# Kernel tuning notes

Hardware: AMD Instinct MI355X
Metric: run time of the kernel (lower is better)

Reference implementation:

```python
import jax, jax.numpy as jnp
import numpy as np

R, H, K, C = 8, 8, 4096, 128  # residual stages, subvectors, codebook size, subvector dim
B, S = 2, 2048


def setup_inputs() -> dict:
    key = jax.random.key(0)
    k1, k2 = jax.random.split(key)
    x = jax.random.normal(k1, (B, S, H * C), dtype=jnp.float32)
    codebook = jax.random.normal(k2, (R, H, K, C), dtype=jnp.float32) * 0.1
    return {"x": x, "codebook": codebook}


def _encode(x, codebook):
    b, s, f = x.shape
    # x.view(b,s,8,2,64).transpose(3,4).flatten(2)  -> interleave the two 64-dim halves per head
    xp = x.reshape(b, s, 8, 2, 64).transpose(0, 1, 2, 4, 3).reshape(b, s, f)
    prescale = jnp.linalg.norm(xp, axis=-1, keepdims=True)  # (b,s,1)
    xn = xp / prescale
    # (b s) h c  -> permute to (h, N, c)
    t0 = xn.reshape(b * s, H, C).transpose(1, 0, 2)  # (H, N, C)

    def step(t, cb_r):
        # cb_r: (H, K, C). Squared-euclidean argmin == torch.cdist argmin (sqrt is monotone,
        # and the ||t||^2 term is constant over k so it is dropped).
        d = jnp.sum(cb_r * cb_r, axis=-1)[:, None, :] - 2.0 * jnp.einsum('hnc,hkc->hnk', t, cb_r)
        idx = jnp.argmin(d, axis=-1)  # (H, N)
        q = jnp.take_along_axis(cb_r, idx[..., None], axis=1)  # (H, N, C)
        return t - q, idx.astype(jnp.int32)

    _, codes = jax.lax.scan(step, t0, codebook)  # codes: (R, H, N)
    return codes, prescale


def _decode(codes, prescale, codebook):
    # gather codebook entries: (R, H, N, C)
    g = jnp.take_along_axis(codebook, codes[..., None], axis=2)
    n = codes.shape[2]
    # permute(0,2,1,3).flatten(-2).sum(0): (R,N,H*C) summed over residual stages
    rec = g.transpose(0, 2, 1, 3).reshape(R, n, H * C).sum(0)  # (N, H*C)
    b = prescale.shape[0]
    return rec.reshape(b, -1, H * C) * prescale


def reference(x, codebook):
    codes, prescale = _encode(x, codebook)
    return _decode(codes, prescale, codebook)
```

## Files before the change

kernel.cpp:

```cpp
#include <hip/hip_runtime.h>

#define R_STAGES 8
#define H_HEADS  8
#define K_CODES  4096
#define C_DIM    128
#define N_TOK    4096
#define FEAT     1024
#define HKC      (H_HEADS * K_CODES * C_DIM)

#define MARGIN   1.2e-2f
#define WCAP     384
#define TMS      260
#define NTILE    64
#define NPH      (K_CODES / NTILE)
#define TPB      64

typedef _Float16 half8  __attribute__((ext_vector_type(8)));
typedef _Float16 half4v __attribute__((ext_vector_type(4)));
typedef float    f32x4  __attribute__((ext_vector_type(4)));

#define MFMA16(A, B, C) __builtin_amdgcn_mfma_f32_16x16x32_f16((A), (B), (C), 0, 0, 0)

__device__ __forceinline__ void glds16(const _Float16* g, _Float16* l) {
    __builtin_amdgcn_global_load_lds(
        (const __attribute__((address_space(1))) void*)g,
        (__attribute__((address_space(3))) void*)l, 16, 0, 0);
}


__global__ void kc_prep(const float* __restrict__ x, float* __restrict__ t,
                        float* __restrict__ ps) {
    int n = blockIdx.x;
    const float* xr = x + (size_t)n * FEAT;

    double ss = 0.0;
    for (int i = threadIdx.x; i < FEAT; i += 256) {
        float v = xr[i];
        ss += (double)v * (double)v;
    }
    for (int off = 32; off > 0; off >>= 1) ss += __shfl_down(ss, off);

    __shared__ double sred[4];
    __shared__ float s_p;
    int wid = threadIdx.x >> 6, lane = threadIdx.x & 63;
    if (lane == 0) sred[wid] = ss;
    __syncthreads();
    if (threadIdx.x == 0) {
        double tot = sred[0] + sred[1] + sred[2] + sred[3];
        float p = (float)sqrt(tot);
        ps[n] = p;
        s_p = p;
    }
    __syncthreads();
    float p = s_p;

    for (int i = threadIdx.x; i < FEAT; i += 256) {
        int c = i & 127;
        float v = xr[(i & ~127) + ((c & 1) << 6) + (c >> 1)];
        size_t o = ((size_t)(i >> 7) * N_TOK + n) * C_DIM + c;
        t[o] = v / p;
    }
}

__global__ void kc_cvtn(const float* __restrict__ cb, _Float16* __restrict__ cb16,
                        float* __restrict__ cn) {
    int w = (blockIdx.x << 2) + (threadIdx.x >> 6);
    int lane = threadIdx.x & 63;
    const float* row = cb + (size_t)w * C_DIM;
    float a = row[lane], b = row[lane + 64];
    _Float16* dr = cb16 + (size_t)w * C_DIM;
    dr[lane]      = (_Float16)a;
    dr[lane + 64] = (_Float16)b;
    double s = (double)a * a + (double)b * b;
    for (int off = 32; off > 0; off >>= 1) s += __shfl_down(s, off);
    if (lane == 0) cn[w] = (float)s;
}

__device__ __forceinline__ void stage_body(
    const float* __restrict__ cbh32, const _Float16* __restrict__ cbh16,
    const float* __restrict__ cnh, float* __restrict__ th) {

    __shared__ __align__(16) _Float16 buf[2][NTILE * C_DIM];
    __shared__ __align__(16) _Float16 tmin[TPB * TMS];
    __shared__ float    mtok[TPB];
    __shared__ int      wl[WCAP];
    __shared__ double   eD[WCAP];
    __shared__ int      eI[WCAP];
    __shared__ int      winner[TPB];
    __shared__ int      wlCnt;

    const int tid  = threadIdx.x;
    const int w    = tid >> 6;
    const int lane = tid & 63;
    const int col  = lane & 15;
    const int rblk = lane >> 4;
    const int tok  = (w << 4) + col;

    if (tid == 0) wlCnt = 0;

    half8 tf[4];
    {
        const float* trow = th + (size_t)tok * C_DIM;
#pragma unroll
        for (int j = 0; j < 4; ++j) {
            const float* p = trow + j * 32 + rblk * 8;
            f32x4 lo = *(const f32x4*)p;
            f32x4 hi = *(const f32x4*)(p + 4);
            half8 v;
            v[0] = (_Float16)lo[0]; v[1] = (_Float16)lo[1];
            v[2] = (_Float16)lo[2]; v[3] = (_Float16)lo[3];
            v[4] = (_Float16)hi[0]; v[5] = (_Float16)hi[1];
            v[6] = (_Float16)hi[2]; v[7] = (_Float16)hi[3];
            tf[j] = v;
        }
    }

    auto stageT = [&](int p, int bsel) {
        const char* gt = (const char*)cbh16 + (size_t)p * (NTILE * 256);
        _Float16* lb = buf[bsel];
#pragma unroll
        for (int i = 0; i < 4; ++i) {
            const int base = (w << 12) + (i << 10);
            const int d    = base + (lane << 4);
            const int src  = d ^ (((d >> 8) & 15) << 4);
            glds16((const _Float16*)(gt + src), lb + (base >> 1));
        }
    };

    float rb = 3.4e38f;

    auto computeT = [&](int p, int bsel) {
        const _Float16* bp = buf[bsel];
        const float* cpp = cnh + p * NTILE + (rblk << 2);
        f32x4 cv[4];
        cv[0] = *(const f32x4*)cpp;
        cv[1] = *(const f32x4*)(cpp + 16);
        cv[2] = *(const f32x4*)(cpp + 32);
        cv[3] = *(const f32x4*)(cpp + 48);
#pragma unroll
        for (int sub = 0; sub < 4; ++sub) {
            const int row  = (sub << 4) + col;
            const int base = (row << 8) + (rblk << 4);
            const int swz  = (row & 15) << 4;
            f32x4 acc = {0.f, 0.f, 0.f, 0.f};
#pragma unroll
            for (int j = 0; j < 4; ++j) {
                half8 A = *(const half8*)(bp + (((base + (j << 6)) ^ swz) >> 1));
                acc = MFMA16(A, tf[j], acc);
            }
            float m = fminf(fminf(cv[sub][0] - 2.f * acc[0], cv[sub][1] - 2.f * acc[1]),
                            fminf(cv[sub][2] - 2.f * acc[2], cv[sub][3] - 2.f * acc[3]));
            float tm = fminf(m, __shfl_xor(m, 16));
            tm = fminf(tm, __shfl_xor(tm, 32));
            rb = fminf(rb, tm);
            if (rblk == 0) tmin[tok * TMS + (p << 2) + sub] = (_Float16)tm;
        }
    };

    stageT(0, 0);
    __syncthreads();
#pragma unroll 1
    for (int p = 0; p < NPH; ++p) {
        if (p + 1 < NPH) stageT(p + 1, (p + 1) & 1);
        computeT(p, p & 1);
        __syncthreads();
    }

    if (rblk == 0) mtok[tok] = rb;
    __syncthreads();

    {
        const int tk = tid >> 2, q = tid & 3;
        const float thr = mtok[tk] + MARGIN;
        const half4v* rowp = (const half4v*)(tmin + tk * TMS + (q << 6));
#pragma unroll 4
        for (int j4 = 0; j4 < 16; ++j4) {
            half4v v = rowp[j4];
#pragma unroll
            for (int e = 0; e < 4; ++e) {
                if ((float)v[e] < thr) {
                    int idx = atomicAdd(&wlCnt, 1);
                    if (idx < WCAP) wl[idx] = (tk << 8) | ((q << 6) + (j4 << 2) + e);
                }
            }
        }
    }
    __syncthreads();

    int E = wlCnt;
    if (E <= WCAP) {
        for (int e0 = 0; e0 < E; e0 += 16) {
            const int e = e0 + (tid >> 4);
            double bd = 1e300; int bi = 0x7fffffff;
            if (e < E) {
                const int meta = wl[e];
                const int tk = meta >> 8;
                const int k = ((meta & 255) << 4) + (tid & 15);
                const float* crow = cbh32 + (size_t)k * C_DIM;
                const float* trw  = th + (size_t)tk * C_DIM;
                double cx0=0,cx1=0,cx2=0,cx3=0,d0=0,d1=0,d2=0,d3=0;
#pragma unroll 4
                for (int c = 0; c < C_DIM; c += 4) {
                    double cv0 = crow[c],   tv0 = trw[c];
                    double cv1 = crow[c+1], tv1 = trw[c+1];
                    double cv2 = crow[c+2], tv2 = trw[c+2];
                    double cv3 = crow[c+3], tv3 = trw[c+3];
                    cx0 = fma(cv0,cv0,cx0); d0 = fma(tv0,cv0,d0);
                    cx1 = fma(cv1,cv1,cx1); d1 = fma(tv1,cv1,d1);
                    cx2 = fma(cv2,cv2,cx2); d2 = fma(tv2,cv2,d2);
                    cx3 = fma(cv3,cv3,cx3); d3 = fma(tv3,cv3,d3);
                }
                bd = ((cx0+cx1)+(cx2+cx3)) - 2.0*((d0+d1)+(d2+d3));
                bi = k;
            }
#pragma unroll
            for (int off = 1; off < 16; off <<= 1) {
                double od = __shfl_xor(bd, off);
                int    oi = __shfl_xor(bi, off);
                if (od < bd || (od == bd && oi < bi)) { bd = od; bi = oi; }
            }
            if ((tid & 15) == 0 && e < E) { eD[e] = bd; eI[e] = bi; }
        }
        __syncthreads();
        if (tid < TPB) {
            double bd = 1e300; int bi = 0x7fffffff;
            for (int e = 0; e < E; ++e) {
                if ((wl[e] >> 8) == tid) {
                    double d = eD[e]; int i2 = eI[e];
                    if (d < bd || (d == bd && i2 < bi)) { bd = d; bi = i2; }
                }
            }
            winner[tid] = bi;
        }
        __syncthreads();
    } else {
        for (int ot = 0; ot < TPB; ++ot) {
            const float* trw = th + (size_t)ot * C_DIM;
            double bd = 1e300; int bi = 0x7fffffff;
            for (int k = tid; k < K_CODES; k += 256) {
                const float* crow = cbh32 + (size_t)k * C_DIM;
                double cx0=0,cx1=0,cx2=0,cx3=0,d0=0,d1=0,d2=0,d3=0;
                for (int c = 0; c < C_DIM; c += 4) {
                    double cv0 = crow[c],   tv0 = trw[c];
                    double cv1 = crow[c+1], tv1 = trw[c+1];
                    double cv2 = crow[c+2], tv2 = trw[c+2];
                    double cv3 = crow[c+3], tv3 = trw[c+3];
                    cx0 = fma(cv0,cv0,cx0); d0 = fma(tv0,cv0,d0);
                    cx1 = fma(cv1,cv1,cx1); d1 = fma(tv1,cv1,d1);
                    cx2 = fma(cv2,cv2,cx2); d2 = fma(tv2,cv2,d2);
                    cx3 = fma(cv3,cv3,cx3); d3 = fma(tv3,cv3,d3);
                }
                double d = ((cx0+cx1)+(cx2+cx3)) - 2.0*((d0+d1)+(d2+d3));
                if (d < bd || (d == bd && k < bi)) { bd = d; bi = k; }
            }
            for (int off = 1; off <= 32; off <<= 1) {
                double od = __shfl_xor(bd, off);
                int    oi = __shfl_xor(bi, off);
                if (od < bd || (od == bd && oi < bi)) { bd = od; bi = oi; }
            }
            if (lane == 0) { eD[w] = bd; eI[w] = bi; }
            __syncthreads();
            if (tid == 0) {
                double b2 = eD[0]; int i2 = eI[0];
                for (int q = 1; q < 4; ++q) {
                    if (eD[q] < b2 || (eD[q] == b2 && eI[q] < i2)) { b2 = eD[q]; i2 = eI[q]; }
                }
                winner[ot] = i2;
            }
            __syncthreads();
        }
    }

    for (int i = tid; i < TPB * C_DIM; i += 256) {
        const int tk = i >> 7, c = i & 127;
        th[(size_t)tk * C_DIM + c] -= cbh32[(size_t)winner[tk] * C_DIM + c];
    }
    __syncthreads();
}

__global__ __launch_bounds__(256, 2)
void kc_all(const float* __restrict__ cb32, const _Float16* __restrict__ cb16,
            const float* __restrict__ cn, float* __restrict__ t) {
    const int h  = blockIdx.x & 7;
    const int n0 = (blockIdx.x >> 3) * TPB;
    float* th = t + ((size_t)h * N_TOK + n0) * C_DIM;
#pragma unroll 1
    for (int r = 0; r < R_STAGES; ++r) {
        const size_t off = (size_t)(r * H_HEADS + h) * K_CODES;
        stage_body(cb32 + off * C_DIM, cb16 + off * C_DIM, cn + off, th);
    }
}

__global__ __launch_bounds__(256, 2)
void kc_stage_one(const float* __restrict__ cb32, const _Float16* __restrict__ cb16,
                  const float* __restrict__ cn, float* __restrict__ t) {
    const int h  = blockIdx.x & 7;
    const int n0 = (blockIdx.x >> 3) * TPB;
    float* th = t + ((size_t)h * N_TOK + n0) * C_DIM;
    const size_t off = (size_t)h * K_CODES;
    stage_body(cb32 + off * C_DIM, cb16 + off * C_DIM, cn + off, th);
}

__global__ void kc_out(const float* __restrict__ x, const float* __restrict__ t,
                       const float* __restrict__ ps, float* __restrict__ out) {
    int n = blockIdx.x;
    float p = ps[n];
    const float* xr = x + (size_t)n * FEAT;
    for (int i = threadIdx.x; i < FEAT; i += 256) {
        int c = i & 127;
        float v = xr[(i & ~127) + ((c & 1) << 6) + (c >> 1)];
        float t0 = v / p;
        float tf = t[((size_t)(i >> 7) * N_TOK + n) * C_DIM + c];
        out[(size_t)n * FEAT + i] = (t0 - tf) * p;
    }
}

extern "C" void kernel_launch(void* const* d_in, const int* in_sizes, int n_in,
                              void* d_out, int out_size, void* d_ws, size_t ws_size,
                              hipStream_t stream) {
    const float* x  = (const float*)d_in[0];
    const float* cb = (const float*)d_in[1];
    float* out = (float*)d_out;

    float*    t    = (float*)d_ws;
    float*    ps   = (float*)((char*)d_ws + 16777216);
    float*    cn   = (float*)((char*)d_ws + 16793600);
    _Float16* cb16 = (_Float16*)((char*)d_ws + 17842176);

    const bool full = (ws_size >= 84951040ull);

    kc_prep<<<N_TOK, 256, 0, stream>>>(x, t, ps);

    if (full) {
        kc_cvtn<<<(R_STAGES * H_HEADS * K_CODES) / 4, 256, 0, stream>>>(cb, cb16, cn);
        kc_all<<<H_HEADS * (N_TOK / TPB), 256, 0, stream>>>(cb, cb16, cn, t);
    } else {
        for (int r = 0; r < R_STAGES; ++r) {
            kc_cvtn<<<(H_HEADS * K_CODES) / 4, 256, 0, stream>>>(
                cb + (size_t)r * HKC, cb16, cn + (size_t)r * H_HEADS * K_CODES);
            kc_stage_one<<<H_HEADS * (N_TOK / TPB), 256, 0, stream>>>(
                cb + (size_t)r * HKC, cb16, cn + (size_t)r * H_HEADS * K_CODES, t);
        }
    }

    kc_out<<<N_TOK, 256, 0, stream>>>(x, t, ps, out);
}
```

Baseline: 1.148 ms.

## Double block size to 512 threads, splitting codebook tiles across wave pairs

Each block now runs 8 waves instead of 4. Waves are split into 4 token groups times 2 codebook halves, so each wave computes half the 64-code tile per phase and issues half the LDS staging loads. Per-token minima from the two halves are merged through a small shared array. The candidate scan, refinement and fallback loops are resized for 512 threads, and the candidate list capacity drops to 256. The aim is more waves in flight to hide MFMA and LDS latency. In exchange, a smaller candidate cap sends more blocks to the slow fallback path, and larger blocks may reduce how many blocks fit per CU.

```diff
diff --git a/kernel.cpp b/kernel.cpp
--- a/kernel.cpp
+++ b/kernel.cpp
@@ -9,11 +9,12 @@
 #define HKC      (H_HEADS * K_CODES * C_DIM)
 
 #define MARGIN   1.2e-2f
-#define WCAP     384
+#define WCAP     256
 #define TMS      260
 #define NTILE    64
 #define NPH      (K_CODES / NTILE)
 #define TPB      64
+#define THREADS  512
 
 typedef _Float16 half8  __attribute__((ext_vector_type(8)));
 typedef _Float16 half4v __attribute__((ext_vector_type(4)));
@@ -82,6 +83,7 @@
 
     __shared__ __align__(16) _Float16 buf[2][NTILE * C_DIM];
     __shared__ __align__(16) _Float16 tmin[TPB * TMS];
+    __shared__ float    rbs[8][16];
     __shared__ float    mtok[TPB];
     __shared__ int      wl[WCAP];
     __shared__ double   eD[WCAP];
@@ -94,7 +96,9 @@
     const int lane = tid & 63;
     const int col  = lane & 15;
     const int rblk = lane >> 4;
-    const int tok  = (w << 4) + col;
+    const int tg   = w & 3;
+    const int kh   = w >> 2;
+    const int tok  = (tg << 4) + col;
 
     if (tid == 0) wlCnt = 0;
 
@@ -119,8 +123,8 @@
         const char* gt = (const char*)cbh16 + (size_t)p * (NTILE * 256);
         _Float16* lb = buf[bsel];
 #pragma unroll
-        for (int i = 0; i < 4; ++i) {
-            const int base = (w << 12) + (i << 10);
+        for (int i = 0; i < 2; ++i) {
+            const int base = (w << 11) + (i << 10);
             const int d    = base + (lane << 4);
             const int src  = d ^ (((d >> 8) & 15) << 4);
             glds16((const _Float16*)(gt + src), lb + (base >> 1));
@@ -131,29 +135,28 @@
 
     auto computeT = [&](int p, int bsel) {
         const _Float16* bp = buf[bsel];
-        const float* cpp = cnh + p * NTILE + (rblk << 2);
-        f32x4 cv[4];
-        cv[0] = *(const f32x4*)cpp;
-        cv[1] = *(const f32x4*)(cpp + 16);
-        cv[2] = *(const f32x4*)(cpp + 32);
-        cv[3] = *(const f32x4*)(cpp + 48);
-#pragma unroll
-        for (int sub = 0; sub < 4; ++sub) {
-            const int row  = (sub << 4) + col;
+        const float* cpp = cnh + p * NTILE + (kh << 5) + (rblk << 2);
+        f32x4 cv0 = *(const f32x4*)cpp;
+        f32x4 cv1 = *(const f32x4*)(cpp + 16);
+#pragma unroll
+        for (int s = 0; s < 2; ++s) {
+            const int row  = (kh << 5) + (s << 4) + col;
             const int base = (row << 8) + (rblk << 4);
-            const int swz  = (row & 15) << 4;
+            const int swz  = col << 4;
             f32x4 acc = {0.f, 0.f, 0.f, 0.f};
 #pragma unroll
             for (int j = 0; j < 4; ++j) {
                 half8 A = *(const half8*)(bp + (((base + (j << 6)) ^ swz) >> 1));
                 acc = MFMA16(A, tf[j], acc);
             }
-            float m = fminf(fminf(cv[sub][0] - 2.f * acc[0], cv[sub][1] - 2.f * acc[1]),
-                            fminf(cv[sub][2] - 2.f * acc[2], cv[sub][3] - 2.f * acc[3]));
+            const f32x4 cv = s ? cv1 : cv0;
+            float m = fminf(fminf(cv[0] - 2.f * acc[0], cv[1] - 2.f * acc[1]),
+                            fminf(cv[2] - 2.f * acc[2], cv[3] - 2.f * acc[3]));
             float tm = fminf(m, __shfl_xor(m, 16));
             tm = fminf(tm, __shfl_xor(tm, 32));
             rb = fminf(rb, tm);
-            if (rblk == 0) tmin[tok * TMS + (p << 2) + sub] = (_Float16)tm;
+            if (rblk == 0)
+                tmin[tok * TMS + (p << 2) + (kh << 1) + s] = (_Float16)tm;
         }
     };
 
@@ -166,21 +169,26 @@
         __syncthreads();
     }
 
-    if (rblk == 0) mtok[tok] = rb;
+    if (rblk == 0) rbs[w][col] = rb;
+    __syncthreads();
+    if (tid < TPB) {
+        const int g = tid >> 4, c2 = tid & 15;
+        mtok[tid] = fminf(rbs[g][c2], rbs[g + 4][c2]);
+    }
     __syncthreads();
 
     {
-        const int tk = tid >> 2, q = tid & 3;
+        const int tk = tid >> 3, q = tid & 7;
         const float thr = mtok[tk] + MARGIN;
-        const half4v* rowp = (const half4v*)(tmin + tk * TMS + (q << 6));
-#pragma unroll 4
-        for (int j4 = 0; j4 < 16; ++j4) {
+        const half4v* rowp = (const half4v*)(tmin + tk * TMS + (q << 5));
+#pragma unroll 2
+        for (int j4 = 0; j4 < 8; ++j4) {
             half4v v = rowp[j4];
 #pragma unroll
             for (int e = 0; e < 4; ++e) {
                 if ((float)v[e] < thr) {
                     int idx = atomicAdd(&wlCnt, 1);
-                    if (idx < WCAP) wl[idx] = (tk << 8) | ((q << 6) + (j4 << 2) + e);
+                    if (idx < WCAP) wl[idx] = (tk << 8) | ((q << 5) + (j4 << 2) + e);
                 }
             }
         }
@@ -189,7 +197,7 @@
 
     int E = wlCnt;
     if (E <= WCAP) {
-        for (int e0 = 0; e0 < E; e0 += 16) {
+        for (int e0 = 0; e0 < E; e0 += 32) {
             const int e = e0 + (tid >> 4);
             double bd = 1e300; int bi = 0x7fffffff;
             if (e < E) {
@@ -237,7 +245,7 @@
         for (int ot = 0; ot < TPB; ++ot) {
             const float* trw = th + (size_t)ot * C_DIM;
             double bd = 1e300; int bi = 0x7fffffff;
-            for (int k = tid; k < K_CODES; k += 256) {
+            for (int k = tid; k < K_CODES; k += THREADS) {
                 const float* crow = cbh32 + (size_t)k * C_DIM;
                 double cx0=0,cx1=0,cx2=0,cx3=0,d0=0,d1=0,d2=0,d3=0;
                 for (int c = 0; c < C_DIM; c += 4) {
@@ -262,7 +270,7 @@
             __syncthreads();
             if (tid == 0) {
                 double b2 = eD[0]; int i2 = eI[0];
-                for (int q = 1; q < 4; ++q) {
+                for (int q = 1; q < 8; ++q) {
                     if (eD[q] < b2 || (eD[q] == b2 && eI[q] < i2)) { b2 = eD[q]; i2 = eI[q]; }
                 }
                 winner[ot] = i2;
@@ -271,14 +279,14 @@
         }
     }
 
-    for (int i = tid; i < TPB * C_DIM; i += 256) {
+    for (int i = tid; i < TPB * C_DIM; i += THREADS) {
         const int tk = i >> 7, c = i & 127;
         th[(size_t)tk * C_DIM + c] -= cbh32[(size_t)winner[tk] * C_DIM + c];
     }
     __syncthreads();
 }
 
-__global__ __launch_bounds__(256, 2)
+__global__ __launch_bounds__(THREADS, 2)
 void kc_all(const float* __restrict__ cb32, const _Float16* __restrict__ cb16,
             const float* __restrict__ cn, float* __restrict__ t) {
     const int h  = blockIdx.x & 7;
@@ -291,7 +299,7 @@
     }
 }
 
-__global__ __launch_bounds__(256, 2)
+__global__ __launch_bounds__(THREADS, 2)
 void kc_stage_one(const float* __restrict__ cb32, const _Float16* __restrict__ cb16,
                   const float* __restrict__ cn, float* __restrict__ t) {
     const int h  = blockIdx.x & 7;
@@ -333,12 +341,12 @@
 
     if (full) {
         kc_cvtn<<<(R_STAGES * H_HEADS * K_CODES) / 4, 256, 0, stream>>>(cb, cb16, cn);
-        kc_all<<<H_HEADS * (N_TOK / TPB), 256, 0, stream>>>(cb, cb16, cn, t);
+        kc_all<<<H_HEADS * (N_TOK / TPB), THREADS, 0, stream>>>(cb, cb16, cn, t);
     } else {
         for (int r = 0; r < R_STAGES; ++r) {
             kc_cvtn<<<(H_HEADS * K_CODES) / 4, 256, 0, stream>>>(
                 cb + (size_t)r * HKC, cb16, cn + (size_t)r * H_HEADS * K_CODES);
-            kc_stage_one<<<H_HEADS * (N_TOK / TPB), 256, 0, stream>>>(
+            kc_stage_one<<<H_HEADS * (N_TOK / TPB), THREADS, 0, stream>>>(
                 cb + (size_t)r * HKC, cb16, cn + (size_t)r * H_HEADS * K_CODES, t);
         }
     }
```

New measurement: 1.577 ms. +37.4%, slower.
